# Kernel tuning notes

Measured on AMD Instinct MI355X. Metric: run time of the kernel, lower is better.

Reference implementation:

```python
import jax, jax.numpy as jnp
import numpy as np

CUTOFF = 6.0
PMAX = 256
RBF_DIM = 32
MAX_Z = 90
Z_EMB = 32


def _mlp(x, layers):
    # layers: list of (W, b); SiLU between all but last
    for W, b in layers[:-1]:
        x = jax.nn.silu(x @ W + b)
    W, b = layers[-1]
    return x @ W + b


def _rbf(r):
    centers = jnp.linspace(0.0, CUTOFF, RBF_DIM)
    delta = CUTOFF / (RBF_DIM - 1)
    gamma = 1.0 / (delta * delta + 1e-12)
    return jnp.exp(-gamma * (r[..., None] - centers) ** 2)


def _cutoff_fn(r):
    return 0.5 * (jnp.cos(jnp.pi * r / CUTOFF) + 1.0) * (r <= CUTOFF).astype(r.dtype)


def setup_inputs() -> dict:
    key = jax.random.key(0)
    ks = jax.random.split(key, 24)
    B, N, H, nE, dE = 16, 64, 128, 128, 32
    inp = {
        'h': jax.random.normal(ks[0], (B, N, H), jnp.float32),
        'z': jax.random.randint(ks[1], (B, N), 1, MAX_Z, dtype=jnp.int32).astype(jnp.int64),
        'pos': jax.random.normal(ks[2], (B, N, 3), jnp.float32) * 2.0,
        'mask': jnp.ones((B, N), dtype=bool),
        'e_feat': jax.random.normal(ks[3], (nE, dE), jnp.float32),
    }
    s = 0.05
    # pair-element MLP: in = 2*Z_EMB + dE = 96 -> 128 -> 128 -> 64
    inp['z_emb'] = jax.random.normal(ks[4], (MAX_Z + 1, Z_EMB), jnp.float32) * s
    inp['pw0'] = jax.random.normal(ks[5], (96, 128), jnp.float32) * s
    inp['pb0'] = jnp.zeros((128,), jnp.float32)
    inp['pw1'] = jax.random.normal(ks[6], (128, 128), jnp.float32) * s
    inp['pb1'] = jnp.zeros((128,), jnp.float32)
    inp['pw2'] = jax.random.normal(ks[7], (128, 64), jnp.float32) * s
    inp['pb2'] = jnp.zeros((64,), jnp.float32)
    # geom MLP: in = 2*128 + 3*32 + 1 = 353 -> 256 -> 256 -> 64
    inp['gw0'] = jax.random.normal(ks[8], (353, 256), jnp.float32) * s
    inp['gb0'] = jnp.zeros((256,), jnp.float32)
    inp['gw1'] = jax.random.normal(ks[9], (256, 256), jnp.float32) * s
    inp['gb1'] = jnp.zeros((256,), jnp.float32)
    inp['gw2'] = jax.random.normal(ks[10], (256, 64), jnp.float32) * s
    inp['gb2'] = jnp.zeros((64,), jnp.float32)
    # out proj: 64 -> 256 -> 128
    inp['ow0'] = jax.random.normal(ks[11], (64, 256), jnp.float32) * s
    inp['ob0'] = jnp.zeros((256,), jnp.float32)
    inp['ow1'] = jax.random.normal(ks[12], (256, 128), jnp.float32) * s
    inp['ob1'] = jnp.zeros((128,), jnp.float32)
    return inp


def _forward(h, pos, e_feat, z_emb, pw0, pb0, pw1, pb1, pw2, pb2,
             gw0, gb0, gw1, gb1, gw2, gb2, ow0, ob0, ow1, ob1, z, mask):
    B, N, H = h.shape
    # absorber-relative geometry (absorber_index = 0)
    rel = pos - pos[:, 0:1, :]                     # [B,N,3]
    r = jnp.linalg.norm(rel, axis=-1)              # [B,N]
    valid = mask & (jnp.arange(N) != 0)[None, :] & (r <= CUTOFF)
    # vectorized triplet-path enumeration: all j<k pairs, sort by score, keep PMAX
    jU, kU = np.triu_indices(N, k=1)               # [M]
    jU = jnp.asarray(jU); kU = jnp.asarray(kU)
    pair_valid = valid[:, jU] & valid[:, kU]       # [B,M]
    r0j_all = r[:, jU]
    r0k_all = r[:, kU]
    rjk_all = jnp.linalg.norm(pos[:, kU] - pos[:, jU], axis=-1)
    score = r0j_all + r0k_all + 0.5 * rjk_all
    score = jnp.where(pair_valid, score, jnp.inf)
    order = jnp.argsort(score, axis=1)[:, :PMAX]   # [B,PMAX]
    pmask = jnp.take_along_axis(pair_valid, order, axis=1)
    j_idx = jnp.where(pmask, jU[order], 0)         # [B,PMAX]
    k_idx = jnp.where(pmask, kU[order], 0)
    # gather features / positions
    hj = jnp.take_along_axis(h, j_idx[:, :, None], axis=1)     # [B,P,H]
    hk = jnp.take_along_axis(h, k_idx[:, :, None], axis=1)
    posj = jnp.take_along_axis(pos, j_idx[:, :, None], axis=1)  # [B,P,3]
    posk = jnp.take_along_axis(pos, k_idx[:, :, None], axis=1)
    pos0 = pos[:, 0:1, :]
    vj = posj - pos0
    vk = posk - pos0
    vjk = posk - posj
    r0j = jnp.linalg.norm(vj, axis=-1)
    r0k = jnp.linalg.norm(vk, axis=-1)
    rjk = jnp.linalg.norm(vjk, axis=-1)
    uj = vj / jnp.maximum(r0j[..., None], 1e-8)
    uk = vk / jnp.maximum(r0k[..., None], 1e-8)
    cosang = jnp.clip(jnp.sum(uj * uk, axis=-1, keepdims=True), -1.0, 1.0)
    f0j = _rbf(jnp.minimum(r0j, CUTOFF))
    f0k = _rbf(jnp.minimum(r0k, CUTOFF))
    fjk = _rbf(jnp.minimum(rjk, CUTOFF))
    geom_in = jnp.concatenate([hj, hk, f0j, f0k, fjk, cosang], axis=-1)  # [B,P,353]
    g_geom = _mlp(geom_in, [(gw0, gb0), (gw1, gb1), (gw2, gb2)])         # [B,P,S]
    # pair-element energy scattering
    P = PMAX
    nE, dE = e_feat.shape
    zj = jnp.take_along_axis(z, j_idx, axis=1)
    zk = jnp.take_along_axis(z, k_idx, axis=1)
    ej = jnp.broadcast_to(z_emb[zj][:, :, None, :], (B, P, nE, Z_EMB))
    ek = jnp.broadcast_to(z_emb[zk][:, :, None, :], (B, P, nE, Z_EMB))
    ef = jnp.broadcast_to(e_feat[None, None, :, :], (B, P, nE, dE))
    pe_in = jnp.concatenate([ej, ek, ef], axis=-1)                       # [B,P,nE,96]
    g_elem = _mlp(pe_in, [(pw0, pb0), (pw1, pb1), (pw2, pb2)])           # [B,P,nE,S]
    # cutoff weighting + masked mean over paths
    cw = _cutoff_fn(r0j) * _cutoff_fn(r0k) * _cutoff_fn(rjk)             # [B,P]
    w = cw * pmask.astype(cw.dtype)                                      # [B,P]
    contrib = g_geom[:, :, None, :] * g_elem * w[:, :, None, None]
    agg = contrib.sum(axis=1)                                            # [B,nE,S]
    norm = jnp.maximum(w.sum(axis=1), 1e-8)[:, None, None]               # [B,1,1]
    agg = agg / norm
    return _mlp(agg, [(ow0, ob0), (ow1, ob1)])                           # [B,nE,out]


def reference(h, z, pos, mask, e_feat, z_emb, pw0, pb0, pw1, pb1, pw2, pb2,
              gw0, gb0, gw1, gb1, gw2, gb2, ow0, ob0, ow1, ob1):
    return _forward(h, pos, e_feat, z_emb, pw0, pb0, pw1, pb1, pw2, pb2,
                    gw0, gb0, gw1, gb1, gw2, gb2, ow0, ob0, ow1, ob1, z, mask)
```

## Files before the change

### kernel.cpp

```cpp
#include <hip/hip_runtime.h>
#include <math.h>

#define NB 16
#define NA 64
#define NPAIR 2016
#define PSEL 256
#define NEL 128
#define WS_SUMW   0
#define WS_SELJ   2048
#define WS_SELK   (WS_SELJ + 16384)
#define WS_SCAL   (WS_SELK + 16384)
#define WS_AE     (WS_SCAL + 131072)
#define WS_GG     (WS_AE + 65536)
#define WS_ZRJ    (WS_GG + 1048576)
#define WS_ZRK    (WS_ZRJ + 47104)
#define WS_AGG    (WS_ZRK + 47104)
#define WS_W1F    (WS_AGG + 524288)
#define WS_W2F    (WS_W1F + 32768)
#define WS_G0F    (WS_W2F + 16384)
#define WS_G1F    (WS_G0F + 196608)
#define WS_G2F    (WS_G1F + 131072)

#define PREP_BLOCKS 1467
#define IDX_W1F  16384
#define IDX_W2F  24576
#define IDX_G0F  122880
#define IDX_G1F  188416
#define IDX_G2F  204800
#define IDX_AE   221184
#define IDX_ZRJ  232832
#define IDX_ZRK  244480
#define IDX_AGG  375552

typedef short v8s __attribute__((ext_vector_type(8)));
typedef float v4f __attribute__((ext_vector_type(4)));

__device__ __forceinline__ float siluf_fast(float x) {
  float e = __expf(-x);
  return x * __builtin_amdgcn_rcpf(1.0f + e);
}
__device__ __forceinline__ unsigned short f2bf(float f) {
  unsigned int u = __float_as_uint(f);
  return (unsigned short)((u + 0x7fffu + ((u >> 16) & 1u)) >> 16);
}
__device__ __forceinline__ unsigned int pk_bf16(float fa, float fb) {
  unsigned int ua = __float_as_uint(fa), ub = __float_as_uint(fb);
  ua = ua + 0x7fffu + ((ua >> 16) & 1u);
  ub = ub + 0x7fffu + ((ub >> 16) & 1u);
  return __builtin_amdgcn_perm(ub, ua, 0x07060302u);
}
__device__ __forceinline__ float cutf(float r) {
  return (r <= 6.0f) ? (0.5f * (cosf((3.14159265358979323846f * r) / 6.0f) + 1.0f)) : 0.0f;
}
__device__ __forceinline__ float rbff(float r, int i) {
  float rc = fminf(r, 6.0f);
  float c = (float)i * (6.0f / 31.0f);
  float d = rc - c;
  return expf(-26.694445f * d * d);
}
__device__ __forceinline__ void pair_jk(int p, int& j, int& k) {
  int jj = (int)((127.0 - sqrt(16129.0 - 8.0 * (double)p)) * 0.5);
  if (jj < 0) jj = 0;
  if (jj > 62) jj = 62;
  while (jj < 62 && (63 * (jj + 1) - ((jj + 1) * jj) / 2) <= p) jj++;
  while (jj > 0 && (63 * jj - (jj * (jj - 1)) / 2) > p) jj--;
  j = jj;
  k = p - (63 * jj - (jj * (jj - 1)) / 2) + jj + 1;
}

__global__ __launch_bounds__(256) void kA(
    const int* __restrict__ z, const float* __restrict__ ef,
    const float* __restrict__ pos,
    const float* __restrict__ pw0, const float* __restrict__ pb0,
    const float* __restrict__ pw1, const float* __restrict__ pw2,
    const float* __restrict__ gw0, const float* __restrict__ gw1,
    const float* __restrict__ gw2, const float* __restrict__ zemb, char* ws) {
  __shared__ float px[64], py[64], pz[64], rr[64];
  __shared__ int hist[256], scan[256];
  __shared__ unsigned long long selk[256];
  __shared__ float wred[256];
  __shared__ unsigned long long s_pref, s_kstar;
  __shared__ int s_K, s_done, s_digit, s_exc, s_cnt;
  int blk = blockIdx.x, t = threadIdx.x;

  if (blk < PREP_BLOCKS) {
    int idx = blk * 256 + t;
    if (idx < IDX_W1F) {
      int j = idx & 7, l = (idx >> 3) & 63, t2 = idx >> 9;
      int kk = t2 & 3, nt = t2 >> 2;
      int n = 16 * nt + (l & 15), k = 32 * kk + (l >> 4) * 8 + j;
      ((unsigned short*)(ws + WS_W1F))[idx] = f2bf(pw1[k * 128 + n]);
    } else if (idx < IDX_W2F) {
      int id = idx - IDX_W1F;
      int j = id & 7, l = (id >> 3) & 63, t2 = id >> 9;
      int kk = t2 & 3, nt = t2 >> 2;
      int n = 16 * nt + (l & 15), k = 32 * kk + (l >> 4) * 8 + j;
      ((unsigned short*)(ws + WS_W2F))[id] = f2bf(pw2[k * 64 + n]);
    } else if (idx < IDX_G0F) {
      int id = idx - IDX_W2F;
      int j = id & 7, l = (id >> 3) & 63, t2 = id >> 9;
      int kk = t2 % 12, nt = t2 / 12;
      int n = 16 * nt + (l & 15), k = 32 * kk + (l >> 4) * 8 + j;
      float v = (k < 353) ? gw0[k * 256 + n] : 0.0f;
      ((unsigned short*)(ws + WS_G0F))[id] = f2bf(v);
    } else if (idx < IDX_G1F) {
      int id = idx - IDX_G0F;
      int j = id & 7, l = (id >> 3) & 63, t2 = id >> 9;
      int kk = t2 & 7, nt = t2 >> 3;
      int n = 16 * nt + (l & 15), k = 32 * kk + (l >> 4) * 8 + j;
      ((unsigned short*)(ws + WS_G1F))[id] = f2bf(gw1[k * 256 + n]);
    } else if (idx < IDX_G2F) {
      int id = idx - IDX_G1F;
      int j = id & 7, l = (id >> 3) & 63, t2 = id >> 9;
      int kk = t2 & 7, nt = t2 >> 3;
      int n = 16 * nt + (l & 15), k = 32 * kk + (l >> 4) * 8 + j;
      ((unsigned short*)(ws + WS_G2F))[id] = f2bf(gw2[k * 64 + n]);
    } else if (idx < IDX_AE) {
      int id = idx - IDX_G2F;
      int e = id >> 7, d = id & 127;
      float a = pb0[d];
      for (int i = 0; i < 32; i++) a += ef[e * 32 + i] * pw0[(64 + i) * 128 + d];
      ((float*)(ws + WS_AE))[e * 128 + d] = a;
    } else if (idx < IDX_ZRJ) {
      int id = idx - IDX_AE;
      int zv = id >> 7, d = id & 127;
      float a = 0.0f;
      for (int i = 0; i < 32; i++) a += zemb[zv * 32 + i] * pw0[i * 128 + d];
      ((float*)(ws + WS_ZRJ))[id] = a;
    } else if (idx < IDX_ZRK) {
      int id = idx - IDX_ZRJ;
      int zv = id >> 7, d = id & 127;
      float a = 0.0f;
      for (int i = 0; i < 32; i++) a += zemb[zv * 32 + i] * pw0[(32 + i) * 128 + d];
      ((float*)(ws + WS_ZRK))[id] = a;
    } else if (idx < IDX_AGG) {
      ((float*)(ws + WS_AGG))[idx - IDX_ZRK] = 0.0f;
    }
    return;
  }

  {
#pragma clang fp contract(off)
    int b = blk - PREP_BLOCKS;
    int is64 = (z[1] == 0) ? 1 : 0;
    if (t < 64) {
      px[t] = pos[(b * 64 + t) * 3 + 0];
      py[t] = pos[(b * 64 + t) * 3 + 1];
      pz[t] = pos[(b * 64 + t) * 3 + 2];
    }
    if (t == 0) { s_pref = 0; s_K = PSEL; s_done = 0; s_cnt = 0; }
    __syncthreads();
    if (t < 64) {
      float dx = px[t] - px[0], dy = py[t] - py[0], dz = pz[t] - pz[0];
      rr[t] = sqrtf((dx * dx + dy * dy) + dz * dz);
    }
    __syncthreads();
    unsigned long long keys[8];
#pragma unroll
    for (int ii = 0; ii < 8; ii++) {
      int p = t + 256 * ii;
      unsigned long long key = 0xFFFFFFFFFFFFFFFFull;
      if (p < NPAIR) {
        int j, k;
        pair_jk(p, j, k);
        bool vj = (j != 0) && (rr[j] <= 6.0f);
        bool vk = (rr[k] <= 6.0f);
        unsigned int sb = 0x7f800000u;
        if (vj && vk) {
          float dx = px[k] - px[j], dy = py[k] - py[j], dz = pz[k] - pz[j];
          float rjk = sqrtf((dx * dx + dy * dy) + dz * dz);
          float score = (rr[j] + rr[k]) + 0.5f * rjk;
          sb = __float_as_uint(score);
        }
        key = (((unsigned long long)sb) << 32) | (unsigned int)p;
      }
      keys[ii] = key;
    }
    for (int shift = 56; shift >= 0; shift -= 8) {
      if (s_done) break;
      hist[t] = 0;
      __syncthreads();
      unsigned long long hiMask = (shift == 56) ? 0ull : (~0ull << (shift + 8));
      unsigned long long pref = s_pref;
      int K = s_K;
#pragma unroll
      for (int ii = 0; ii < 8; ii++) {
        if ((keys[ii] & hiMask) == pref)
          atomicAdd(&hist[(int)((keys[ii] >> shift) & 255)], 1);
      }
      __syncthreads();
      scan[t] = hist[t];
      __syncthreads();
      for (int off = 1; off < 256; off <<= 1) {
        int add = (t >= off) ? scan[t - off] : 0;
        __syncthreads();
        scan[t] += add;
        __syncthreads();
      }
      int inc = scan[t], exc = inc - hist[t];
      if (exc < K && K <= inc) { s_digit = t; s_exc = exc; }
      __syncthreads();
      int d = s_digit, exc2 = s_exc, cnt = hist[d];
      unsigned long long npref = pref | ((unsigned long long)d << shift);
      if (cnt == 1) {
        unsigned long long inclMask = hiMask | (255ull << shift);
#pragma unroll
        for (int ii = 0; ii < 8; ii++)
          if ((keys[ii] & inclMask) == npref) s_kstar = keys[ii];
        if (t == 0) s_done = 1;
      } else if (shift == 0) {
        if (t == 0) { s_kstar = npref; s_done = 1; }
      } else {
        if (t == 0) { s_pref = npref; s_K = K - exc2; }
      }
      __syncthreads();
    }
    unsigned long long kstar = s_kstar;
#pragma unroll
    for (int ii = 0; ii < 8; ii++) {
      if (keys[ii] <= kstar) {
        int slot = atomicAdd(&s_cnt, 1);
        selk[slot] = keys[ii];
      }
    }
    __syncthreads();
    float myw = 0.0f;
    {
      unsigned long long key = selk[t];
      unsigned int sb = (unsigned int)(key >> 32);
      int p = (int)(key & 0xFFFFFFFFu);
      bool pv = (sb < 0x7f800000u);
      int j = 0, k = 0;
      if (pv) pair_jk(p, j, k);
      float r0j = rr[j], r0k = rr[k];
      float vjx = px[j] - px[0], vjy = py[j] - py[0], vjz = pz[j] - pz[0];
      float vkx = px[k] - px[0], vky = py[k] - py[0], vkz = pz[k] - pz[0];
      float dx = px[k] - px[j], dy = py[k] - py[j], dz = pz[k] - pz[j];
      float rjk = sqrtf((dx * dx + dy * dy) + dz * dz);
      float ij = 1.0f / fmaxf(r0j, 1e-8f);
      float ik = 1.0f / fmaxf(r0k, 1e-8f);
      float cs = (vjx * vkx + vjy * vky + vjz * vkz) * ij * ik;
      cs = fminf(1.0f, fmaxf(-1.0f, cs));
      float w = pv ? (cutf(r0j) * cutf(r0k) * cutf(rjk)) : 0.0f;
      int zj = is64 ? z[(b * 64 + j) * 2] : z[b * 64 + j];
      int zk = is64 ? z[(b * 64 + k) * 2] : z[b * 64 + k];
      int* selJ = (int*)(ws + WS_SELJ);
      int* selK = (int*)(ws + WS_SELK);
      float* scal = (float*)(ws + WS_SCAL);
      selJ[b * PSEL + t] = j;
      selK[b * PSEL + t] = k;
      float* s = &scal[(b * PSEL + t) * 8];
      s[0] = r0j; s[1] = r0k; s[2] = rjk; s[3] = cs; s[4] = w;
      ((int*)s)[5] = zj; ((int*)s)[6] = zk;
      myw = w;
    }
    wred[t] = myw;
    __syncthreads();
    for (int s2 = 128; s2 > 0; s2 >>= 1) {
      if (t < s2) wred[t] += wred[t + s2];
      __syncthreads();
    }
    if (t == 0) ((float*)(ws + WS_SUMW))[b] = fmaxf(wred[0], 1e-8f);
  }
}

#define LP3 392
#define LQ3 264
__global__ __launch_bounds__(256) void k3_geom(const float* __restrict__ h,
    const float* __restrict__ gb0, const float* __restrict__ gb1,
    const float* __restrict__ gb2, char* ws) {
  int blk = blockIdx.x;
  int b = blk >> 4, p0 = (blk & 15) * 16;
  int t = threadIdx.x;
  int lane = t & 63, w = t >> 6;
  int q = lane >> 4, m4 = lane & 15;
  const int* selJ = (const int*)(ws + WS_SELJ);
  const int* selK = (const int*)(ws + WS_SELK);
  const float* scal = (const float*)(ws + WS_SCAL);
  const float* sumw = (const float*)(ws + WS_SUMW);
  float* gg = (float*)(ws + WS_GG);
  const unsigned short* G0F = (const unsigned short*)(ws + WS_G0F);
  const unsigned short* G1F = (const unsigned short*)(ws + WS_G1F);
  const unsigned short* G2F = (const unsigned short*)(ws + WS_G2F);
  __shared__ __align__(16) unsigned short xs[16 * LP3];
  __shared__ __align__(16) unsigned short x1s[16 * LQ3];
  __shared__ __align__(16) unsigned short x2s[16 * LQ3];
  const v4f z4 = {0.f, 0.f, 0.f, 0.f};
  {
    int row = t & 15, fs = t >> 4;
    int p = p0 + row;
    int j = selJ[b * PSEL + p], k = selK[b * PSEL + p];
    const float* s = &scal[(b * PSEL + p) * 8];
    float r0j = s[0], r0k = s[1], rjk = s[2], cs = s[3];
    for (int f = fs; f < 384; f += 16) {
      float v;
      if (f < 128) v = h[(b * 64 + j) * 128 + f];
      else if (f < 256) v = h[(b * 64 + k) * 128 + (f - 128)];
      else if (f < 288) v = rbff(r0j, f - 256);
      else if (f < 320) v = rbff(r0k, f - 288);
      else if (f < 352) v = rbff(rjk, f - 320);
      else if (f == 352) v = cs;
      else v = 0.0f;
      xs[row * LP3 + f] = f2bf(v);
    }
  }
  __syncthreads();
  {
    v4f acc[4];
#pragma unroll
    for (int nt = 0; nt < 4; nt++) acc[nt] = z4;
    for (int kk = 0; kk < 12; kk++) {
      v8s bf = *(const v8s*)&xs[m4 * LP3 + 32 * kk + 8 * q];
#pragma unroll
      for (int nt = 0; nt < 4; nt++) {
        v8s wf = *(const v8s*)&G0F[(((4 * w + nt) * 12 + kk) * 64 + lane) * 8];
        acc[nt] = __builtin_amdgcn_mfma_f32_16x16x32_bf16(wf, bf, acc[nt], 0, 0, 0);
      }
    }
#pragma unroll
    for (int nt = 0; nt < 4; nt++) {
      int n0 = 64 * w + 16 * nt + 4 * q;
      float4 bias = *(const float4*)&gb0[n0];
      uint2 o;
      o.x = pk_bf16(siluf_fast(acc[nt][0] + bias.x), siluf_fast(acc[nt][1] + bias.y));
      o.y = pk_bf16(siluf_fast(acc[nt][2] + bias.z), siluf_fast(acc[nt][3] + bias.w));
      *(uint2*)&x1s[m4 * LQ3 + n0] = o;
    }
  }
  __syncthreads();
  {
    v4f acc[4];
#pragma unroll
    for (int nt = 0; nt < 4; nt++) acc[nt] = z4;
    for (int kk = 0; kk < 8; kk++) {
      v8s bf = *(const v8s*)&x1s[m4 * LQ3 + 32 * kk + 8 * q];
#pragma unroll
      for (int nt = 0; nt < 4; nt++) {
        v8s wf = *(const v8s*)&G1F[(((4 * w + nt) * 8 + kk) * 64 + lane) * 8];
        acc[nt] = __builtin_amdgcn_mfma_f32_16x16x32_bf16(wf, bf, acc[nt], 0, 0, 0);
      }
    }
#pragma unroll
    for (int nt = 0; nt < 4; nt++) {
      int n0 = 64 * w + 16 * nt + 4 * q;
      float4 bias = *(const float4*)&gb1[n0];
      uint2 o;
      o.x = pk_bf16(siluf_fast(acc[nt][0] + bias.x), siluf_fast(acc[nt][1] + bias.y));
      o.y = pk_bf16(siluf_fast(acc[nt][2] + bias.z), siluf_fast(acc[nt][3] + bias.w));
      *(uint2*)&x2s[m4 * LQ3 + n0] = o;
    }
  }
  __syncthreads();
  {
    v4f acc = z4;
    for (int kk = 0; kk < 8; kk++) {
      v8s bf = *(const v8s*)&x2s[m4 * LQ3 + 32 * kk + 8 * q];
      v8s wf = *(const v8s*)&G2F[((w * 8 + kk) * 64 + lane) * 8];
      acc = __builtin_amdgcn_mfma_f32_16x16x32_bf16(wf, bf, acc, 0, 0, 0);
    }
    int p = p0 + m4;
    float wp = scal[(b * PSEL + p) * 8 + 4];
    float s2 = wp / sumw[b];
    int n0 = 16 * w + 4 * q;
    float4 bias = *(const float4*)&gb2[n0];
    float4 o;
    o.x = (acc[0] + bias.x) * s2;
    o.y = (acc[1] + bias.y) * s2;
    o.z = (acc[2] + bias.z) * s2;
    o.w = (acc[3] + bias.w) * s2;
    *(float4*)&gg[(b * PSEL + p) * 64 + n0] = o;
  }
}

#define LP 136
__global__ __launch_bounds__(256, 4) void k4_elem(
    const float* __restrict__ pb1, const float* __restrict__ pb2, char* ws) {
  int et = blockIdx.x, b = blockIdx.y, pc = blockIdx.z;
  int t = threadIdx.x;
  int lane = t & 63, w = t >> 6;
  int q = lane >> 4, m4 = lane & 15;
  const float* Ae = (const float*)(ws + WS_AE);
  const float* gg = (const float*)(ws + WS_GG);
  const float* zrJ = (const float*)(ws + WS_ZRJ);
  const float* zrK = (const float*)(ws + WS_ZRK);
  const unsigned short* W1F = (const unsigned short*)(ws + WS_W1F);
  const unsigned short* W2F = (const unsigned short*)(ws + WS_W2F);
  float* agg = (float*)(ws + WS_AGG);
  __shared__ __align__(16) unsigned short x0s[64 * LP];
  __shared__ __align__(16) unsigned short x1s[64 * LP];
  int e0 = et * 8;

  v8s w1f[2][4], w2f[4];
#pragma unroll
  for (int ct = 0; ct < 2; ct++)
#pragma unroll
    for (int kk = 0; kk < 4; kk++)
      w1f[ct][kk] = *(const v8s*)&W1F[(((2 * w + ct) * 4 + kk) * 64 + lane) * 8];
#pragma unroll
  for (int kk = 0; kk < 4; kk++)
    w2f[kk] = *(const v8s*)&W2F[(((w) * 4 + kk) * 64 + lane) * 8];
  float4 b1v[2];
  b1v[0] = *(const float4*)&pb1[32 * w + 4 * q];
  b1v[1] = *(const float4*)&pb1[32 * w + 16 + 4 * q];
  float4 b2v = *(const float4*)&pb2[16 * w + 4 * q];

  int pl = t >> 5, k0 = (t & 31) * 4;
  const int* sI = (const int*)(ws + WS_SCAL) + (b * PSEL + pc * 64 + pl) * 8;
  const float* aep = Ae + e0 * 128 + k0;
  unsigned short* xw = &x0s[pl * LP + k0];
  const float* ggp = gg + (b * PSEL + pc * 64 + (lane & 7)) * 64 + 16 * w + 4 * q;

  v4f aggR[4];
  const v4f z4 = {0.f, 0.f, 0.f, 0.f};
#pragma unroll
  for (int mt = 0; mt < 4; mt++) aggR[mt] = z4;

  for (int g2 = 0; g2 < 8; g2++) {
    int zj = sI[5], zk = sI[6];
    sI += 64;
    float4 aj = *(const float4*)&zrJ[zj * 128 + k0];
    float4 ak = *(const float4*)&zrK[zk * 128 + k0];
    float4 a0v;
    a0v.x = aj.x + ak.x; a0v.y = aj.y + ak.y;
    a0v.z = aj.z + ak.z; a0v.w = aj.w + ak.w;
#pragma unroll
    for (int it = 0; it < 8; it++) {
      float4 aev = *(const float4*)(aep + it * 128);
      uint2 o;
      o.x = pk_bf16(siluf_fast(a0v.x + aev.x), siluf_fast(a0v.y + aev.y));
      o.y = pk_bf16(siluf_fast(a0v.z + aev.z), siluf_fast(a0v.w + aev.w));
      *(uint2*)(xw + it * 8 * LP) = o;
    }
    __syncthreads();
    v4f acc1[4][2];
#pragma unroll
    for (int mt = 0; mt < 4; mt++) { acc1[mt][0] = z4; acc1[mt][1] = z4; }
#pragma unroll
    for (int kk = 0; kk < 4; kk++) {
#pragma unroll
      for (int mt = 0; mt < 4; mt++) {
        v8s bf = *(const v8s*)&x0s[(16 * mt + m4) * LP + 32 * kk + 8 * q];
        acc1[mt][0] = __builtin_amdgcn_mfma_f32_16x16x32_bf16(w1f[0][kk], bf, acc1[mt][0], 0, 0, 0);
        acc1[mt][1] = __builtin_amdgcn_mfma_f32_16x16x32_bf16(w1f[1][kk], bf, acc1[mt][1], 0, 0, 0);
      }
    }
#pragma unroll
    for (int mt = 0; mt < 4; mt++) {
#pragma unroll
      for (int ct = 0; ct < 2; ct++) {
        float4 bias = b1v[ct];
        uint2 o;
        o.x = pk_bf16(siluf_fast(acc1[mt][ct][0] + bias.x), siluf_fast(acc1[mt][ct][1] + bias.y));
        o.y = pk_bf16(siluf_fast(acc1[mt][ct][2] + bias.z), siluf_fast(acc1[mt][ct][3] + bias.w));
        int n0 = 32 * w + 16 * ct + 4 * q;
        *(uint2*)&x1s[(16 * mt + m4) * LP + n0] = o;
      }
    }
    __syncthreads();
    v4f acc2[4];
#pragma unroll
    for (int mt = 0; mt < 4; mt++) acc2[mt] = z4;
#pragma unroll
    for (int kk = 0; kk < 4; kk++) {
#pragma unroll
      for (int mt = 0; mt < 4; mt++) {
        v8s bf = *(const v8s*)&x1s[(16 * mt + m4) * LP + 32 * kk + 8 * q];
        acc2[mt] = __builtin_amdgcn_mfma_f32_16x16x32_bf16(w2f[kk], bf, acc2[mt], 0, 0, 0);
      }
    }
    float4 gv = *(const float4*)ggp;
    ggp += 512;
#pragma unroll
    for (int mt = 0; mt < 4; mt++) {
      aggR[mt][0] += gv.x * (acc2[mt][0] + b2v.x);
      aggR[mt][1] += gv.y * (acc2[mt][1] + b2v.y);
      aggR[mt][2] += gv.z * (acc2[mt][2] + b2v.z);
      aggR[mt][3] += gv.w * (acc2[mt][3] + b2v.w);
    }
  }
#pragma unroll
  for (int mt = 0; mt < 4; mt++) {
#pragma unroll
    for (int r = 0; r < 4; r++) {
      float v = aggR[mt][r];
      v += __shfl_xor(v, 1);
      v += __shfl_xor(v, 2);
      v += __shfl_xor(v, 4);
      if ((lane & 7) == 0) {
        int e = 2 * mt + ((lane >> 3) & 1);
        int n = 16 * w + 4 * q + r;
        atomicAdd(&agg[(b * NEL + e0 + e) * 64 + n], v);
      }
    }
  }
}

__global__ __launch_bounds__(256) void k5_out(
    const float* __restrict__ ow0, const float* __restrict__ ob0,
    const float* __restrict__ ow1, const float* __restrict__ ob1,
    const char* ws, float* __restrict__ out) {
  int row0 = blockIdx.x * 16;
  int t = threadIdx.x;
  const float* agg = (const float*)(ws + WS_AGG);
  __shared__ float xT[64][16];
  __shared__ float x1T[256][16];
  {
    int row = t & 15, fs = t >> 4;
    for (int f = fs; f < 64; f += 16) xT[f][row] = agg[(row0 + row) * 64 + f];
  }
  __syncthreads();
  {
    int r0 = (t & 3) * 4, c0 = (t >> 2) * 4;
    float acc[4][4] = {};
    for (int k2 = 0; k2 < 64; k2++) {
      float4 xv = *(const float4*)&xT[k2][r0];
      float4 wv = *(const float4*)&ow0[k2 * 256 + c0];
      float xs2[4] = {xv.x, xv.y, xv.z, xv.w};
      float wss[4] = {wv.x, wv.y, wv.z, wv.w};
#pragma unroll
      for (int i = 0; i < 4; i++)
#pragma unroll
        for (int j2 = 0; j2 < 4; j2++) acc[i][j2] += xs2[i] * wss[j2];
    }
#pragma unroll
    for (int jj = 0; jj < 4; jj++) {
      float bias = ob0[c0 + jj];
#pragma unroll
      for (int i = 0; i < 4; i++) x1T[c0 + jj][r0 + i] = siluf_fast(acc[i][jj] + bias);
    }
  }
  __syncthreads();
  {
    int r0 = (t & 3) * 4, c0 = (t >> 2) * 2;
    float acc[4][2] = {};
    for (int k2 = 0; k2 < 256; k2++) {
      float4 xv = *(const float4*)&x1T[k2][r0];
      float2 wv = *(const float2*)&ow1[k2 * 128 + c0];
      float xs2[4] = {xv.x, xv.y, xv.z, xv.w};
#pragma unroll
      for (int i = 0; i < 4; i++) {
        acc[i][0] += xs2[i] * wv.x;
        acc[i][1] += xs2[i] * wv.y;
      }
    }
#pragma unroll
    for (int i = 0; i < 4; i++)
#pragma unroll
      for (int j2 = 0; j2 < 2; j2++)
        out[(row0 + r0 + i) * 128 + c0 + j2] = acc[i][j2] + ob1[c0 + j2];
  }
}

extern "C" void kernel_launch(void* const* d_in, const int* in_sizes, int n_in,
                              void* d_out, int out_size, void* d_ws, size_t ws_size,
                              hipStream_t stream) {
  const float* h     = (const float*)d_in[0];
  const int*   z     = (const int*)d_in[1];
  const float* pos   = (const float*)d_in[2];
  const float* efeat = (const float*)d_in[4];
  const float* zemb  = (const float*)d_in[5];
  const float* pw0 = (const float*)d_in[6];
  const float* pb0 = (const float*)d_in[7];
  const float* pw1 = (const float*)d_in[8];
  const float* pb1 = (const float*)d_in[9];
  const float* pw2 = (const float*)d_in[10];
  const float* pb2 = (const float*)d_in[11];
  const float* gw0 = (const float*)d_in[12];
  const float* gb0 = (const float*)d_in[13];
  const float* gw1 = (const float*)d_in[14];
  const float* gb1 = (const float*)d_in[15];
  const float* gw2 = (const float*)d_in[16];
  const float* gb2 = (const float*)d_in[17];
  const float* ow0 = (const float*)d_in[18];
  const float* ob0 = (const float*)d_in[19];
  const float* ow1 = (const float*)d_in[20];
  const float* ob1 = (const float*)d_in[21];
  char* ws = (char*)d_ws;
  float* out = (float*)d_out;

  kA<<<PREP_BLOCKS + 16, 256, 0, stream>>>(z, efeat, pos, pw0, pb0, pw1, pw2,
                                           gw0, gw1, gw2, zemb, ws);
  k3_geom<<<256, 256, 0, stream>>>(h, gb0, gb1, gb2, ws);
  k4_elem<<<dim3(16, 16, 4), 256, 0, stream>>>(pb1, pb2, ws);
  k5_out<<<128, 256, 0, stream>>>(ow0, ob0, ow1, ob1, ws, out);
}
```

Before: 216.0 us.

## Fuse output MLP into element kernel via per-batch completion counter

Removes the separate k5_out launch. Each k4_elem block increments a per-batch done counter after its atomic aggregation, and eight designated blocks per batch spin until all 64 blocks have finished, then run the output MLP on 16 rows each. The Ae rows are also hoisted into registers once instead of being reloaded every group iteration. This saves a kernel launch and tail gap, but it relies on the waiting blocks not starving the producer blocks of residency and adds spin-wait latency plus register pressure.

Measured after the change: 274.1 us. 1.27x slower.

```diff
diff --git a/kernel.cpp b/kernel.cpp
--- a/kernel.cpp
+++ b/kernel.cpp
@@ -7,6 +7,7 @@
 #define PSEL 256
 #define NEL 128
 #define WS_SUMW   0
+#define WS_DONE   1024
 #define WS_SELJ   2048
 #define WS_SELK   (WS_SELJ + 16384)
 #define WS_SCAL   (WS_SELK + 16384)
@@ -142,6 +143,7 @@
   {
 #pragma clang fp contract(off)
     int b = blk - PREP_BLOCKS;
+    if (t == 0) *((int*)(ws + WS_DONE + b * 64)) = 0;
     int is64 = (z[1] == 0) ? 1 : 0;
     if (t < 64) {
       px[t] = pos[(b * 64 + t) * 3 + 0];
@@ -374,7 +376,10 @@
 
 #define LP 136
 __global__ __launch_bounds__(256, 4) void k4_elem(
-    const float* __restrict__ pb1, const float* __restrict__ pb2, char* ws) {
+    const float* __restrict__ pb1, const float* __restrict__ pb2,
+    const float* __restrict__ ow0, const float* __restrict__ ob0,
+    const float* __restrict__ ow1, const float* __restrict__ ob1,
+    char* ws, float* __restrict__ out) {
   int et = blockIdx.x, b = blockIdx.y, pc = blockIdx.z;
   int t = threadIdx.x;
   int lane = t & 63, w = t >> 6;
@@ -406,9 +411,15 @@
 
   int pl = t >> 5, k0 = (t & 31) * 4;
   const int* sI = (const int*)(ws + WS_SCAL) + (b * PSEL + pc * 64 + pl) * 8;
-  const float* aep = Ae + e0 * 128 + k0;
   unsigned short* xw = &x0s[pl * LP + k0];
   const float* ggp = gg + (b * PSEL + pc * 64 + (lane & 7)) * 64 + 16 * w + 4 * q;
+
+  float4 ae[8];
+  {
+    const float* aep = Ae + e0 * 128 + k0;
+#pragma unroll
+    for (int it = 0; it < 8; it++) ae[it] = *(const float4*)(aep + it * 128);
+  }
 
   v4f aggR[4];
   const v4f z4 = {0.f, 0.f, 0.f, 0.f};
@@ -425,7 +436,7 @@
     a0v.z = aj.z + ak.z; a0v.w = aj.w + ak.w;
 #pragma unroll
     for (int it = 0; it < 8; it++) {
-      float4 aev = *(const float4*)(aep + it * 128);
+      float4 aev = ae[it];
       uint2 o;
       o.x = pk_bf16(siluf_fast(a0v.x + aev.x), siluf_fast(a0v.y + aev.y));
       o.y = pk_bf16(siluf_fast(a0v.z + aev.z), siluf_fast(a0v.w + aev.w));
@@ -493,61 +504,71 @@
       }
     }
   }
-}
-
-__global__ __launch_bounds__(256) void k5_out(
-    const float* __restrict__ ow0, const float* __restrict__ ob0,
-    const float* __restrict__ ow1, const float* __restrict__ ob1,
-    const char* ws, float* __restrict__ out) {
-  int row0 = blockIdx.x * 16;
-  int t = threadIdx.x;
-  const float* agg = (const float*)(ws + WS_AGG);
-  __shared__ float xT[64][16];
-  __shared__ float x1T[256][16];
-  {
-    int row = t & 15, fs = t >> 4;
-    for (int f = fs; f < 64; f += 16) xT[f][row] = agg[(row0 + row) * 64 + f];
+
+  int* done = (int*)(ws + WS_DONE + b * 64);
+  __syncthreads();
+  if (t == 0)
+    __hip_atomic_fetch_add(done, 1, __ATOMIC_ACQ_REL, __HIP_MEMORY_SCOPE_AGENT);
+  if (!(pc == 0 && et < 8)) return;
+  if (t == 0) {
+    long long spins = 0;
+    while (__hip_atomic_load(done, __ATOMIC_ACQUIRE, __HIP_MEMORY_SCOPE_AGENT) < 64) {
+      __builtin_amdgcn_s_sleep(8);
+      if (++spins > (1ll << 26)) break;
+    }
   }
   __syncthreads();
   {
-    int r0 = (t & 3) * 4, c0 = (t >> 2) * 4;
-    float acc[4][4] = {};
-    for (int k2 = 0; k2 < 64; k2++) {
-      float4 xv = *(const float4*)&xT[k2][r0];
-      float4 wv = *(const float4*)&ow0[k2 * 256 + c0];
-      float xs2[4] = {xv.x, xv.y, xv.z, xv.w};
-      float wss[4] = {wv.x, wv.y, wv.z, wv.w};
+    int row0 = b * 128 + et * 16;
+    float* xT = (float*)x0s;
+    float* x1T = (float*)x1s;
+    {
+      int row = t & 15, fs = t >> 4;
+      for (int f = fs; f < 64; f += 16)
+        xT[f * 16 + row] = __hip_atomic_load(&agg[(row0 + row) * 64 + f],
+                                             __ATOMIC_RELAXED, __HIP_MEMORY_SCOPE_AGENT);
+    }
+    __syncthreads();
+    {
+      int r0 = (t & 3) * 4, c0 = (t >> 2) * 4;
+      float acc[4][4] = {};
+      for (int k2 = 0; k2 < 64; k2++) {
+        float4 xv = *(const float4*)&xT[k2 * 16 + r0];
+        float4 wv = *(const float4*)&ow0[k2 * 256 + c0];
+        float xs2[4] = {xv.x, xv.y, xv.z, xv.w};
+        float wss[4] = {wv.x, wv.y, wv.z, wv.w};
+#pragma unroll
+        for (int i = 0; i < 4; i++)
+#pragma unroll
+          for (int j2 = 0; j2 < 4; j2++) acc[i][j2] += xs2[i] * wss[j2];
+      }
+#pragma unroll
+      for (int jj = 0; jj < 4; jj++) {
+        float bias = ob0[c0 + jj];
+#pragma unroll
+        for (int i = 0; i < 4; i++) x1T[(c0 + jj) * 16 + r0 + i] = siluf_fast(acc[i][jj] + bias);
+      }
+    }
+    __syncthreads();
+    {
+      int r0 = (t & 3) * 4, c0 = (t >> 2) * 2;
+      float acc[4][2] = {};
+      for (int k2 = 0; k2 < 256; k2++) {
+        float4 xv = *(const float4*)&x1T[k2 * 16 + r0];
+        float2 wv = *(const float2*)&ow1[k2 * 128 + c0];
+        float xs2[4] = {xv.x, xv.y, xv.z, xv.w};
+#pragma unroll
+        for (int i = 0; i < 4; i++) {
+          acc[i][0] += xs2[i] * wv.x;
+          acc[i][1] += xs2[i] * wv.y;
+        }
+      }
 #pragma unroll
       for (int i = 0; i < 4; i++)
 #pragma unroll
-        for (int j2 = 0; j2 < 4; j2++) acc[i][j2] += xs2[i] * wss[j2];
-    }
-#pragma unroll
-    for (int jj = 0; jj < 4; jj++) {
-      float bias = ob0[c0 + jj];
-#pragma unroll
-      for (int i = 0; i < 4; i++) x1T[c0 + jj][r0 + i] = siluf_fast(acc[i][jj] + bias);
-    }
-  }
-  __syncthreads();
-  {
-    int r0 = (t & 3) * 4, c0 = (t >> 2) * 2;
-    float acc[4][2] = {};
-    for (int k2 = 0; k2 < 256; k2++) {
-      float4 xv = *(const float4*)&x1T[k2][r0];
-      float2 wv = *(const float2*)&ow1[k2 * 128 + c0];
-      float xs2[4] = {xv.x, xv.y, xv.z, xv.w};
-#pragma unroll
-      for (int i = 0; i < 4; i++) {
-        acc[i][0] += xs2[i] * wv.x;
-        acc[i][1] += xs2[i] * wv.y;
-      }
-    }
-#pragma unroll
-    for (int i = 0; i < 4; i++)
-#pragma unroll
-      for (int j2 = 0; j2 < 2; j2++)
-        out[(row0 + r0 + i) * 128 + c0 + j2] = acc[i][j2] + ob1[c0 + j2];
+        for (int j2 = 0; j2 < 2; j2++)
+          out[(row0 + r0 + i) * 128 + c0 + j2] = acc[i][j2] + ob1[c0 + j2];
+    }
   }
 }
 
@@ -581,6 +602,5 @@
   kA<<<PREP_BLOCKS + 16, 256, 0, stream>>>(z, efeat, pos, pw0, pb0, pw1, pw2,
                                            gw0, gw1, gw2, zemb, ws);
   k3_geom<<<256, 256, 0, stream>>>(h, gb0, gb1, gb2, ws);
-  k4_elem<<<dim3(16, 16, 4), 256, 0, stream>>>(pb1, pb2, ws);
-  k5_out<<<128, 256, 0, stream>>>(ow0, ob0, ow1, ob1, ws, out);
-}
+  k4_elem<<<dim3(16, 16, 4), 256, 0, stream>>>(pb1, pb2, ow0, ob0, ow1, ob1, ws, out);
+}
```
